# Performance work log

Measured on AMD Instinct MI355X. Metric: run time of the kernel, lower is better.

The kernel has to match this reference:

```python
import jax, jax.numpy as jnp
import numpy as np

B, N, D, H = 4, 4096, 512, 8
K = D // H  # per-head dim = 64


def setup_inputs() -> dict:
    key = jax.random.key(0)
    k1, k2, k3, k4 = jax.random.split(key, 4)
    x = jax.random.normal(k1, (B, N, D), dtype=jnp.float32)
    # Conv1d(D, K, 1, bias=False) -> weight matrix [K, D], kaiming fan_out
    Wa = jax.random.normal(k2, (K, D), dtype=jnp.float32) * np.float32(np.sqrt(2.0 / K))
    # Conv1d(K, 1, 1) -> weight vector [K], bias scalar (init 0.01)
    Wb = jax.random.normal(k3, (K,), dtype=jnp.float32) * np.float32(np.sqrt(2.0))
    Wc = jax.random.normal(k4, (K,), dtype=jnp.float32) * np.float32(np.sqrt(2.0))
    wb_bias = jnp.full((), 0.01, dtype=jnp.float32)
    wc_bias = jnp.full((), 0.01, dtype=jnp.float32)
    bias = jnp.full((K,), 0.01, dtype=jnp.float32)
    return {"batchinput": x, "Wa": Wa, "Wb": Wb, "wb_bias": wb_bias,
            "Wc": Wc, "wc_bias": wc_bias, "bias": bias}


def reference(batchinput, Wa, Wb, wb_bias, Wc, wc_bias, bias):
    # single step (n_steps=1); all n_head heads share weights, so mean over
    # identical heads equals one head (dropout=0.0 -> identity).
    h = jnp.einsum('bnd,kd->bnk', batchinput, Wa)            # [B,N,K] projected feats
    t1 = jnp.einsum('bnk,k->bn', h, Wb) + wb_bias            # [B,N]
    t2 = jnp.einsum('bnk,k->bn', h, Wc) + wc_bias            # [B,N]
    scores = t1[:, :, None] + t2[:, None, :]                 # [B,N,N] additive score
    coefs = jax.nn.softmax(jax.nn.leaky_relu(scores, negative_slope=0.2), axis=-1)
    out = jnp.einsum('bnm,bmk->bnk', coefs, h) + bias        # [B,N,K]
    return out
```

## Files before the change

kernel.cpp:

```cpp
#include <hip/hip_runtime.h>
#include <hip/hip_bf16.h>

constexpr int cB = 4;
constexpr int cN = 4096;
constexpr int cD = 512;
constexpr int cK = 64;
constexpr int cNB = cB * cN;
constexpr int cNP = cN + 1;
constexpr int cCS = 16;
constexpr int cNC = cN / cCS;
constexpr int cNC1 = cNC + 1;

typedef unsigned short u16;
typedef unsigned int u32;
typedef unsigned long long u64;
typedef __bf16 bf16x8 __attribute__((ext_vector_type(8)));
typedef float f32x4 __attribute__((ext_vector_type(4)));

constexpr size_t OFF_H    = 0;
constexpr size_t OFF_T1   = OFF_H    + (size_t)cNB * cK;
constexpr size_t OFF_T2   = OFF_T1   + cNB;
constexpr size_t OFF_T2S  = OFF_T2   + cNB;
constexpr size_t OFF_IDX  = OFF_T2S  + cNB;
constexpr size_t OFF_EPL  = OFF_IDX  + cNB;
constexpr size_t OFF_GNL  = OFF_EPL  + (size_t)cB * cNP * cK;
constexpr size_t OFF_EPS  = OFF_GNL  + (size_t)cB * cNP * cK;
constexpr size_t OFF_GNS  = OFF_EPS  + (size_t)cB * cNP;
constexpr size_t OFF_CHE  = OFF_GNS  + (size_t)cB * cNP;
constexpr size_t OFF_CHG  = OFF_CHE  + (size_t)cB * cNC * cK;
constexpr size_t OFF_CHES = OFF_CHG  + (size_t)cB * cNC * cK;
constexpr size_t OFF_CHGS = OFF_CHES + (size_t)cB * cNC;
constexpr size_t OFF_OFE  = OFF_CHGS + (size_t)cB * cNC;
constexpr size_t OFF_OFG  = OFF_OFE  + (size_t)cB * cNC1 * cK;
constexpr size_t OFF_OFES = OFF_OFG  + (size_t)cB * cNC1 * cK;
constexpr size_t OFF_OFGS = OFF_OFES + (size_t)cB * cNC1;
constexpr size_t OFF_XB16 = OFF_OFGS + (size_t)cB * cNC1;
constexpr size_t OFF_WB16 = OFF_XB16 + (size_t)cNB * cD / 2;

__device__ __forceinline__ u16 f2bf(float f) {
    unsigned u = __float_as_uint(f);
    u += 0x7fffu + ((u >> 16) & 1u);
    return (u16)(u >> 16);
}
__device__ __forceinline__ u32 pk2(float a, float b) {
    return (u32)f2bf(a) | ((u32)f2bf(b) << 16);
}
__device__ __forceinline__ u32 f2sort(float f) {
    u32 b = __float_as_uint(f);
    u32 mask = (u32)((int)b >> 31);
    return b ^ (mask | 0x80000000u);
}

__global__ __launch_bounds__(256) void k_prep(
    const float* __restrict__ x, const float* __restrict__ Wa,
    const float* __restrict__ Wb, const float* __restrict__ wbb,
    const float* __restrict__ Wc, const float* __restrict__ wcb,
    u16* __restrict__ xb16, u16* __restrict__ wab16,
    float* __restrict__ t1, float* __restrict__ t2)
{
    __shared__ float wabL[cD], wacL[cD];
    int t = threadIdx.x;
    if (blockIdx.x >= 512) {
        int i4 = (((int)blockIdx.x - 512) * 256 + t) * 4;
        float4 v = *(const float4*)(Wa + i4);
        uint2 p = {pk2(v.x, v.y), pk2(v.z, v.w)};
        *(uint2*)(wab16 + i4) = p;
        return;
    }
    float s1a = 0.f, s2a = 0.f, s1b = 0.f, s2b = 0.f;
#pragma unroll 8
    for (int k = 0; k < cK; ++k) {
        float wbk = Wb[k], wck = Wc[k];
        float wa1 = Wa[k * cD + t];
        float wa2 = Wa[k * cD + t + 256];
        s1a += wa1 * wbk; s2a += wa1 * wck;
        s1b += wa2 * wbk; s2b += wa2 * wck;
    }
    wabL[t] = s1a; wacL[t] = s2a; wabL[t + 256] = s1b; wacL[t + 256] = s2b;
    __syncthreads();

    int w = t >> 6, lane = t & 63;
    int d1 = lane * 4, d2 = 256 + lane * 4;
    float4 wbA = *(const float4*)&wabL[d1], wbB = *(const float4*)&wabL[d2];
    float4 wcA = *(const float4*)&wacL[d1], wcB = *(const float4*)&wacL[d2];
    float wbbv = wbb[0], wcbv = wcb[0];
#pragma unroll 2
    for (int rr = 0; rr < 8; ++rr) {
        int row = blockIdx.x * 32 + w * 8 + rr;
        const float* xp = x + (size_t)row * cD;
        float4 a  = *(const float4*)(xp + d1);
        float4 bq = *(const float4*)(xp + d2);
        uint2 pa = {pk2(a.x, a.y), pk2(a.z, a.w)};
        uint2 pb = {pk2(bq.x, bq.y), pk2(bq.z, bq.w)};
        *(uint2*)(xb16 + (size_t)row * cD + d1) = pa;
        *(uint2*)(xb16 + (size_t)row * cD + d2) = pb;
        float p1 = a.x*wbA.x + a.y*wbA.y + a.z*wbA.z + a.w*wbA.w
                 + bq.x*wbB.x + bq.y*wbB.y + bq.z*wbB.z + bq.w*wbB.w;
        float p2 = a.x*wcA.x + a.y*wcA.y + a.z*wcA.z + a.w*wcA.w
                 + bq.x*wcB.x + bq.y*wcB.y + bq.z*wcB.z + bq.w*wcB.w;
#pragma unroll
        for (int off = 32; off > 0; off >>= 1) {
            p1 += __shfl_down(p1, off, 64);
            p2 += __shfl_down(p2, off, 64);
        }
        if (lane == 0) { t1[row] = p1 + wbbv; t2[row] = p2 + wcbv; }
    }
}

__global__ __launch_bounds__(256) void k_projrank(
    const u16* __restrict__ xb16, const u16* __restrict__ wab16,
    const float* __restrict__ t2,
    float* __restrict__ h, float* __restrict__ t2s, int* __restrict__ idxs)
{
    __shared__ u64 shbuf[4096 + 128];
    int t = threadIdx.x;
    if (blockIdx.x < 256) {
        u16* xs = (u16*)shbuf;
        u16* was = xs + 64 * 32;
        int rowbase = blockIdx.x * 64;
        int w = t >> 6, lane = t & 63, m = lane & 15, quad = lane >> 4;
        int grow = w * 16 + (lane >> 2);
        int gcol = (lane & 3) * 8;
        const u16* xg = xb16 + (size_t)(rowbase + grow) * cD + gcol;
        const u16* wg = wab16 + (size_t)grow * cD + gcol;
        int lidx = grow * 32 + gcol;

        f32x4 acc[4] = {{0.f,0.f,0.f,0.f},{0.f,0.f,0.f,0.f},
                        {0.f,0.f,0.f,0.f},{0.f,0.f,0.f,0.f}};
        uint4 xv = *(const uint4*)(xg);
        uint4 wv = *(const uint4*)(wg);
        for (int s = 0; s < 16; ++s) {
            __syncthreads();
            *(uint4*)&xs[lidx] = xv;
            *(uint4*)&was[lidx] = wv;
            if (s < 15) {
                xv = *(const uint4*)(xg + (s + 1) * 32);
                wv = *(const uint4*)(wg + (s + 1) * 32);
            }
            __syncthreads();
            bf16x8 av = *(const bf16x8*)&xs[(w * 16 + m) * 32 + quad * 8];
#pragma unroll
            for (int g = 0; g < 4; ++g) {
                bf16x8 bv = *(const bf16x8*)&was[(g * 16 + m) * 32 + quad * 8];
                acc[g] = __builtin_amdgcn_mfma_f32_16x16x32_bf16(av, bv, acc[g], 0, 0, 0);
            }
        }
#pragma unroll
        for (int g = 0; g < 4; ++g) {
#pragma unroll
            for (int r4 = 0; r4 < 4; ++r4) {
                int row = w * 16 + quad * 4 + r4;
                h[(size_t)(rowbase + row) * cK + g * 16 + m] = acc[g][r4];
            }
        }
    } else {
        u64* keys = shbuf;
        int* part = (int*)(shbuf + 4096);
        int rb = blockIdx.x - 256;
        int b = rb >> 6;
        int rowgrp = rb & 63;
        for (int i = t; i < cN; i += 256)
            keys[i] = ((u64)f2sort(t2[b * cN + i]) << 32) | (u32)i;
        __syncthreads();
        int lane = t & 63, subset = t >> 6;
        u64 mykey = keys[rowgrp * 64 + lane];
        int s0 = subset * 1024;
        int cnt = 0;
#pragma unroll 8
        for (int kk = 0; kk < 1024; ++kk)
            cnt += (keys[s0 + kk] < mykey) ? 1 : 0;
        part[subset * 64 + lane] = cnt;
        __syncthreads();
        if (t < 64) {
            int jj = rowgrp * 64 + t;
            int rank = part[t] + part[64 + t] + part[128 + t] + part[192 + t];
            t2s[b * cN + rank] = t2[b * cN + jj];
            idxs[b * cN + rank] = jj;
        }
    }
}

__global__ __launch_bounds__(64) void k_chunkscan(
    const float* __restrict__ t2s, const int* __restrict__ idxs,
    const float* __restrict__ h,
    float* __restrict__ EpL, float* __restrict__ GnL,
    float* __restrict__ eps_l, float* __restrict__ gns_l,
    float* __restrict__ chE, float* __restrict__ chG,
    float* __restrict__ chEs, float* __restrict__ chGs)
{
    int lane = threadIdx.x;
    int blk = blockIdx.x;
    int c = blk & (cNC - 1);
    int b = blk >> 8;
    int base = b * cN + c * cCS;
    size_t rowbase = ((size_t)b * cNP + c * cCS) * cK;
    int sbase = b * cNP + c * cCS;
    float M2 = t2s[b * cN + cN - 1];
    int   idxv = (lane < cCS) ? idxs[base + lane] : 0;
    float t2v  = (lane < cCS) ? t2s[base + lane] : 0.f;

    float hv[cCS];
#pragma unroll
    for (int i = 0; i < cCS; ++i) {
        int j = __shfl(idxv, i, 64);
        hv[i] = h[((size_t)b * cN + j) * cK + lane];
    }
    float ee[cCS], gg[cCS];
#pragma unroll
    for (int i = 0; i < cCS; ++i) {
        float d = __shfl(t2v, i, 64) - M2;
        ee[i] = __expf(d);
        gg[i] = __expf(0.2f * d);
    }
    if (c == cNC - 1) {
        EpL[((size_t)b * cNP + cN) * cK + lane] = 0.f;
        GnL[((size_t)b * cNP + cN) * cK + lane] = 0.f;
        if (lane == 0) { eps_l[b * cNP + cN] = 0.f; gns_l[b * cNP + cN] = 0.f; }
    }
    float acc = 0.f, accs = 0.f;
#pragma unroll
    for (int i = cCS - 1; i >= 0; --i) {
        acc += ee[i] * hv[i]; accs += ee[i];
        EpL[rowbase + (size_t)i * cK + lane] = acc;
        if (lane == 0) eps_l[sbase + i] = accs;
    }
    chE[((size_t)b * cNC + c) * cK + lane] = acc;
    if (lane == 0) chEs[b * cNC + c] = accs;
    acc = 0.f; accs = 0.f;
#pragma unroll
    for (int i = 0; i < cCS; ++i) {
        GnL[rowbase + (size_t)i * cK + lane] = acc;
        if (lane == 0) gns_l[sbase + i] = accs;
        acc += gg[i] * hv[i]; accs += gg[i];
    }
    chG[((size_t)b * cNC + c) * cK + lane] = acc;
    if (lane == 0) chGs[b * cNC + c] = accs;
}

__global__ __launch_bounds__(256) void k_offsets(
    const float* __restrict__ chE, const float* __restrict__ chG,
    const float* __restrict__ chEs, const float* __restrict__ chGs,
    float* __restrict__ ofE, float* __restrict__ ofG,
    float* __restrict__ ofEs, float* __restrict__ ofGs)
{
    __shared__ float wsum[4][64];
    int t = threadIdx.x;
    int lane = t & 63, w = t >> 6;
    int dir = blockIdx.x & 1;
    int b = blockIdx.x >> 1;
    const float* ch = dir ? chG : chE;
    float* of = dir ? ofG : ofE;
    int c0 = w * 64;

    float cv[64];
    float s = 0.f;
#pragma unroll
    for (int i = 0; i < 64; ++i) {
        cv[i] = ch[((size_t)b * cNC + c0 + i) * cK + lane];
        s += cv[i];
    }
    wsum[w][lane] = s;
    __syncthreads();
    float base = 0.f;
    if (dir == 0) { for (int w2 = w + 1; w2 < 4; ++w2) base += wsum[w2][lane]; }
    else          { for (int w2 = 0; w2 < w; ++w2) base += wsum[w2][lane]; }

    if (dir == 0) {
        float run = base;
#pragma unroll
        for (int i = 63; i >= 0; --i) {
            of[((size_t)b * cNC1 + c0 + i) * cK + lane] = run;
            run += cv[i];
        }
        if (w == 0) of[((size_t)b * cNC1 + cNC) * cK + lane] = 0.f;
    } else {
        float run = base;
#pragma unroll
        for (int i = 0; i < 64; ++i) {
            of[((size_t)b * cNC1 + c0 + i) * cK + lane] = run;
            run += cv[i];
        }
        if (w == 3) of[((size_t)b * cNC1 + cNC) * cK + lane] = run;
    }

    if (w == 0) {
        const float* chs = dir ? chGs : chEs;
        float* ofs = dir ? ofGs : ofEs;
        float e0 = chs[b * cNC + lane * 4 + 0];
        float e1 = chs[b * cNC + lane * 4 + 1];
        float e2 = chs[b * cNC + lane * 4 + 2];
        float e3 = chs[b * cNC + lane * 4 + 3];
        float p = e0 + e1 + e2 + e3;
        if (dir == 0) {
            float s2 = p;
#pragma unroll
            for (int off = 1; off < 64; off <<= 1) {
                float tv = __shfl_down(s2, off, 64);
                if (lane + off < 64) s2 += tv;
            }
            float excl = s2 - p;
            ofs[b * cNC1 + lane * 4 + 0] = excl + e1 + e2 + e3;
            ofs[b * cNC1 + lane * 4 + 1] = excl + e2 + e3;
            ofs[b * cNC1 + lane * 4 + 2] = excl + e3;
            ofs[b * cNC1 + lane * 4 + 3] = excl;
            if (lane == 0) ofs[b * cNC1 + cNC] = 0.f;
        } else {
            float s2 = p;
#pragma unroll
            for (int off = 1; off < 64; off <<= 1) {
                float tv = __shfl_up(s2, off, 64);
                if (lane >= off) s2 += tv;
            }
            float excl = s2 - p;
            ofs[b * cNC1 + lane * 4 + 0] = excl;
            ofs[b * cNC1 + lane * 4 + 1] = excl + e0;
            ofs[b * cNC1 + lane * 4 + 2] = excl + e0 + e1;
            ofs[b * cNC1 + lane * 4 + 3] = excl + e0 + e1 + e2;
            if (lane == 63) ofs[b * cNC1 + cNC] = s2;
        }
    }
}

__global__ __launch_bounds__(256) void k_out(
    const float* __restrict__ t1, const float* __restrict__ t2s,
    const float* __restrict__ EpL, const float* __restrict__ GnL,
    const float* __restrict__ eps_l, const float* __restrict__ gns_l,
    const float* __restrict__ ofE, const float* __restrict__ ofG,
    const float* __restrict__ ofEs, const float* __restrict__ ofGs,
    const float* __restrict__ bias, float* __restrict__ out)
{
    int tid = threadIdx.x;
    int lane = tid & 63;
    int r = blockIdx.x * 4 + (tid >> 6);
    int b = r >> 12;
    float T1 = t1[r];
    float M2 = t2s[b * cN + cN - 1];
    float smax = T1 + M2;
    float m = fmaxf(smax, 0.2f * smax);
    float A  = __expf(smax - m);
    float Cc = __expf(0.2f * smax - m);
    float keyv = -T1;
    int lo = 0, hi = cN;
    while (lo < hi) {
        int mid = (lo + hi) >> 1;
        if (t2s[b * cN + mid] < keyv) lo = mid + 1; else hi = mid;
    }
    int p = lo;
    int c = p >> 4;
    size_t pr = ((size_t)b * cNP + p) * cK + lane;
    size_t cr = ((size_t)b * cNC1 + c) * cK + lane;
    float num = A * (EpL[pr] + ofE[cr]) + Cc * (GnL[pr] + ofG[cr]);
    float den = A * (eps_l[(size_t)b * cNP + p] + ofEs[b * cNC1 + c])
              + Cc * (gns_l[(size_t)b * cNP + p] + ofGs[b * cNC1 + c]);
    out[(size_t)r * cK + lane] = num / den + bias[lane];
}

extern "C" void kernel_launch(void* const* d_in, const int* in_sizes, int n_in,
                              void* d_out, int out_size, void* d_ws, size_t ws_size,
                              hipStream_t stream)
{
    const float* x    = (const float*)d_in[0];
    const float* Wa   = (const float*)d_in[1];
    const float* Wb   = (const float*)d_in[2];
    const float* wbb  = (const float*)d_in[3];
    const float* Wc   = (const float*)d_in[4];
    const float* wcb  = (const float*)d_in[5];
    const float* bias = (const float*)d_in[6];
    float* out = (float*)d_out;

    float* ws = (float*)d_ws;
    float* h     = ws + OFF_H;
    float* t1    = ws + OFF_T1;
    float* t2    = ws + OFF_T2;
    float* t2s   = ws + OFF_T2S;
    int*   idxs  = (int*)(ws + OFF_IDX);
    float* EpL   = ws + OFF_EPL;
    float* GnL   = ws + OFF_GNL;
    float* eps_l = ws + OFF_EPS;
    float* gns_l = ws + OFF_GNS;
    float* chE   = ws + OFF_CHE;
    float* chG   = ws + OFF_CHG;
    float* chEs  = ws + OFF_CHES;
    float* chGs  = ws + OFF_CHGS;
    float* ofE   = ws + OFF_OFE;
    float* ofG   = ws + OFF_OFG;
    float* ofEs  = ws + OFF_OFES;
    float* ofGs  = ws + OFF_OFGS;
    u16*   xb16  = (u16*)(ws + OFF_XB16);
    u16*   wab16 = (u16*)(ws + OFF_WB16);

    k_prep<<<544, 256, 0, stream>>>(x, Wa, Wb, wbb, Wc, wcb, xb16, wab16, t1, t2);
    k_projrank<<<512, 256, 0, stream>>>(xb16, wab16, t2, h, t2s, idxs);
    k_chunkscan<<<cB * cNC, 64, 0, stream>>>(t2s, idxs, h, EpL, GnL, eps_l, gns_l,
                                             chE, chG, chEs, chGs);
    k_offsets<<<cB * 2, 256, 0, stream>>>(chE, chG, chEs, chGs, ofE, ofG, ofEs, ofGs);
    k_out<<<cNB / 4, 256, 0, stream>>>(t1, t2s, EpL, GnL, eps_l, gns_l,
                                       ofE, ofG, ofEs, ofGs, bias, out);
}
```

Before: 132.3 us.

## Compute split positions during rank pass and widen offsets scan block

The rank kernel now also counts, for each row, how many t2 keys fall below -t1, which gives the split position directly. This replaces the per-row binary search over sorted t2 in the output kernel, whose dependent global loads add latency. The offsets kernel now uses 1024 threads with 16 chunks per wave instead of 256 threads with 64, which shortens each thread's serial loop and lowers register pressure. In exchange the rank loop does an extra comparison per key, and equal keys may be tie-broken slightly differently than before.

```diff
diff --git a/kernel.cpp b/kernel.cpp
--- a/kernel.cpp
+++ b/kernel.cpp
@@ -22,7 +22,8 @@
 constexpr size_t OFF_T2   = OFF_T1   + cNB;
 constexpr size_t OFF_T2S  = OFF_T2   + cNB;
 constexpr size_t OFF_IDX  = OFF_T2S  + cNB;
-constexpr size_t OFF_EPL  = OFF_IDX  + cNB;
+constexpr size_t OFF_P    = OFF_IDX  + cNB;
+constexpr size_t OFF_EPL  = OFF_P    + cNB;
 constexpr size_t OFF_GNL  = OFF_EPL  + (size_t)cB * cNP * cK;
 constexpr size_t OFF_EPS  = OFF_GNL  + (size_t)cB * cNP * cK;
 constexpr size_t OFF_GNS  = OFF_EPS  + (size_t)cB * cNP;
@@ -109,10 +110,11 @@
 
 __global__ __launch_bounds__(256) void k_projrank(
     const u16* __restrict__ xb16, const u16* __restrict__ wab16,
-    const float* __restrict__ t2,
-    float* __restrict__ h, float* __restrict__ t2s, int* __restrict__ idxs)
-{
-    __shared__ u64 shbuf[4096 + 128];
+    const float* __restrict__ t1, const float* __restrict__ t2,
+    float* __restrict__ h, float* __restrict__ t2s, int* __restrict__ idxs,
+    int* __restrict__ pidx)
+{
+    __shared__ __align__(16) u64 shbuf[4096 + 256];
     int t = threadIdx.x;
     if (blockIdx.x < 256) {
         u16* xs = (u16*)shbuf;
@@ -163,19 +165,27 @@
             keys[i] = ((u64)f2sort(t2[b * cN + i]) << 32) | (u32)i;
         __syncthreads();
         int lane = t & 63, subset = t >> 6;
-        u64 mykey = keys[rowgrp * 64 + lane];
+        int myrow = rowgrp * 64 + lane;
+        u64 mykey = keys[myrow];
+        u32 pk_hi = f2sort(-t1[(size_t)b * cN + myrow]);
         int s0 = subset * 1024;
-        int cnt = 0;
+        int cnt = 0, cnt2 = 0;
 #pragma unroll 8
-        for (int kk = 0; kk < 1024; ++kk)
-            cnt += (keys[s0 + kk] < mykey) ? 1 : 0;
+        for (int kk = 0; kk < 1024; ++kk) {
+            u64 kv = keys[s0 + kk];
+            cnt  += (kv < mykey) ? 1 : 0;
+            cnt2 += ((u32)(kv >> 32) < pk_hi) ? 1 : 0;
+        }
         part[subset * 64 + lane] = cnt;
+        part[256 + subset * 64 + lane] = cnt2;
         __syncthreads();
         if (t < 64) {
             int jj = rowgrp * 64 + t;
             int rank = part[t] + part[64 + t] + part[128 + t] + part[192 + t];
+            int pc   = part[256 + t] + part[320 + t] + part[384 + t] + part[448 + t];
             t2s[b * cN + rank] = t2[b * cN + jj];
             idxs[b * cN + rank] = jj;
+            pidx[b * cN + jj] = pc;
         }
     }
 }
@@ -237,38 +247,38 @@
     if (lane == 0) chGs[b * cNC + c] = accs;
 }
 
-__global__ __launch_bounds__(256) void k_offsets(
+__global__ __launch_bounds__(1024) void k_offsets(
     const float* __restrict__ chE, const float* __restrict__ chG,
     const float* __restrict__ chEs, const float* __restrict__ chGs,
     float* __restrict__ ofE, float* __restrict__ ofG,
     float* __restrict__ ofEs, float* __restrict__ ofGs)
 {
-    __shared__ float wsum[4][64];
+    __shared__ float wsum[16][64];
     int t = threadIdx.x;
     int lane = t & 63, w = t >> 6;
     int dir = blockIdx.x & 1;
     int b = blockIdx.x >> 1;
     const float* ch = dir ? chG : chE;
     float* of = dir ? ofG : ofE;
-    int c0 = w * 64;
-
-    float cv[64];
+    int c0 = w * 16;
+
+    float cv[16];
     float s = 0.f;
 #pragma unroll
-    for (int i = 0; i < 64; ++i) {
+    for (int i = 0; i < 16; ++i) {
         cv[i] = ch[((size_t)b * cNC + c0 + i) * cK + lane];
         s += cv[i];
     }
     wsum[w][lane] = s;
     __syncthreads();
     float base = 0.f;
-    if (dir == 0) { for (int w2 = w + 1; w2 < 4; ++w2) base += wsum[w2][lane]; }
+    if (dir == 0) { for (int w2 = w + 1; w2 < 16; ++w2) base += wsum[w2][lane]; }
     else          { for (int w2 = 0; w2 < w; ++w2) base += wsum[w2][lane]; }
 
     if (dir == 0) {
         float run = base;
 #pragma unroll
-        for (int i = 63; i >= 0; --i) {
+        for (int i = 15; i >= 0; --i) {
             of[((size_t)b * cNC1 + c0 + i) * cK + lane] = run;
             run += cv[i];
         }
@@ -276,11 +286,11 @@
     } else {
         float run = base;
 #pragma unroll
-        for (int i = 0; i < 64; ++i) {
+        for (int i = 0; i < 16; ++i) {
             of[((size_t)b * cNC1 + c0 + i) * cK + lane] = run;
             run += cv[i];
         }
-        if (w == 3) of[((size_t)b * cNC1 + cNC) * cK + lane] = run;
+        if (w == 15) of[((size_t)b * cNC1 + cNC) * cK + lane] = run;
     }
 
     if (w == 0) {
@@ -323,6 +333,7 @@
 
 __global__ __launch_bounds__(256) void k_out(
     const float* __restrict__ t1, const float* __restrict__ t2s,
+    const int* __restrict__ pidx,
     const float* __restrict__ EpL, const float* __restrict__ GnL,
     const float* __restrict__ eps_l, const float* __restrict__ gns_l,
     const float* __restrict__ ofE, const float* __restrict__ ofG,
@@ -339,13 +350,7 @@
     float m = fmaxf(smax, 0.2f * smax);
     float A  = __expf(smax - m);
     float Cc = __expf(0.2f * smax - m);
-    float keyv = -T1;
-    int lo = 0, hi = cN;
-    while (lo < hi) {
-        int mid = (lo + hi) >> 1;
-        if (t2s[b * cN + mid] < keyv) lo = mid + 1; else hi = mid;
-    }
-    int p = lo;
+    int p = pidx[r];
     int c = p >> 4;
     size_t pr = ((size_t)b * cNP + p) * cK + lane;
     size_t cr = ((size_t)b * cNC1 + c) * cK + lane;
@@ -374,6 +379,7 @@
     float* t2    = ws + OFF_T2;
     float* t2s   = ws + OFF_T2S;
     int*   idxs  = (int*)(ws + OFF_IDX);
+    int*   pidx  = (int*)(ws + OFF_P);
     float* EpL   = ws + OFF_EPL;
     float* GnL   = ws + OFF_GNL;
     float* eps_l = ws + OFF_EPS;
@@ -390,10 +396,10 @@
     u16*   wab16 = (u16*)(ws + OFF_WB16);
 
     k_prep<<<544, 256, 0, stream>>>(x, Wa, Wb, wbb, Wc, wcb, xb16, wab16, t1, t2);
-    k_projrank<<<512, 256, 0, stream>>>(xb16, wab16, t2, h, t2s, idxs);
+    k_projrank<<<512, 256, 0, stream>>>(xb16, wab16, t1, t2, h, t2s, idxs, pidx);
     k_chunkscan<<<cB * cNC, 64, 0, stream>>>(t2s, idxs, h, EpL, GnL, eps_l, gns_l,
                                              chE, chG, chEs, chGs);
-    k_offsets<<<cB * 2, 256, 0, stream>>>(chE, chG, chEs, chGs, ofE, ofG, ofEs, ofGs);
-    k_out<<<cNB / 4, 256, 0, stream>>>(t1, t2s, EpL, GnL, eps_l, gns_l,
+    k_offsets<<<cB * 2, 1024, 0, stream>>>(chE, chG, chEs, chGs, ofE, ofG, ofEs, ofGs);
+    k_out<<<cNB / 4, 256, 0, stream>>>(t1, t2s, pidx, EpL, GnL, eps_l, gns_l,
                                        ofE, ofG, ofEs, ofGs, bias, out);
 }
```

Measured after the change: 130.4 us. No clear change (-1.5%).
